# Optimization experiments

Measured on AMD Instinct MI355X. Metric: run time of the kernel, lower is better.

The kernel has to match this reference:

```python
import jax, jax.numpy as jnp
import numpy as np
import math

NUM_HEADS = 16
VEC_SIZE = 1024
HEAD_DIM = VEC_SIZE // NUM_HEADS


def setup_inputs() -> dict:
    key = jax.random.key(0)
    k1, k2, k3, k4, k5 = jax.random.split(key, 5)
    B, S, D = 2, 2048, VEC_SIZE
    x = jax.random.normal(k1, (B, S, D), dtype=jnp.float32)
    # Linear params, torch-style: y = x @ W.T + b
    s1 = 1.0 / math.sqrt(D)
    W_qkv = jax.random.uniform(k2, (3 * D, D), minval=-s1, maxval=s1, dtype=jnp.float32)
    b_qkv = jax.random.uniform(k3, (3 * D,), minval=-s1, maxval=s1, dtype=jnp.float32)
    W_out = jax.random.uniform(k4, (D, D), minval=-s1, maxval=s1, dtype=jnp.float32)
    b_out = jax.random.uniform(k5, (D,), minval=-s1, maxval=s1, dtype=jnp.float32)
    return {"x": x, "W_qkv": W_qkv, "b_qkv": b_qkv, "W_out": W_out, "b_out": b_out}


def reference(x, W_qkv, b_qkv, W_out, b_out):
    B, S, D = x.shape
    H, Hd = NUM_HEADS, HEAD_DIM
    qkv = x @ W_qkv.T + b_qkv                      # [B,S,3D]
    q, k, v = jnp.split(qkv, 3, axis=-1)
    # [B,S,H,Hd] -> [B,H,S,Hd]
    q = q.reshape(B, S, H, Hd).transpose(0, 2, 1, 3)
    k = k.reshape(B, S, H, Hd).transpose(0, 2, 1, 3)
    v = v.reshape(B, S, H, Hd).transpose(0, 2, 1, 3)
    weight = jnp.einsum('bhqd,bhkd->bhqk', q, k)   # [B,H,S,S]
    causal = jnp.triu(jnp.ones((S, S), dtype=bool), k=1)
    weight = jnp.where(causal, -jnp.inf, weight)
    weight = weight / jnp.sqrt(jnp.asarray(Hd, dtype=weight.dtype))
    weight = jax.nn.softmax(weight, axis=-1)
    out = jnp.einsum('bhqk,bhkd->bhqd', weight, v)  # [B,H,S,Hd]
    out = out.transpose(0, 2, 1, 3).reshape(B, S, D)
    return out @ W_out.T + b_out
```

## Files before the change

kernel.cpp:

```cpp
#include <hip/hip_runtime.h>
#include <hip/hip_bf16.h>

typedef __attribute__((ext_vector_type(8))) short short8;
typedef __attribute__((ext_vector_type(4))) short s4v;
typedef __attribute__((ext_vector_type(4))) float floatx4;

__device__ inline floatx4 mfma_bf16(short8 a, short8 b, floatx4 c) {
  return __builtin_amdgcn_mfma_f32_16x16x32_bf16(a, b, c, 0, 0, 0);
}
__device__ inline float exp2_fast(float x) { return __builtin_amdgcn_exp2f(x); }

__device__ inline short bf16s(float f) {
  __hip_bfloat16 h = __float2bfloat16(f);
  return *reinterpret_cast<short*>(&h);
}
__device__ inline float sbf16(short s) {
  return __bfloat162float(*reinterpret_cast<__hip_bfloat16*>(&s));
}

__device__ inline void gld16(__hip_bfloat16* lds, const __hip_bfloat16* g) {
  __builtin_amdgcn_global_load_lds(
      (const __attribute__((address_space(1))) void*)g,
      (__attribute__((address_space(3))) void*)lds, 16, 0, 0);
}

__global__ __launch_bounds__(256) void cvt_all(
    const float* __restrict__ x, const float* __restrict__ wqkv,
    const float* __restrict__ wout, __hip_bfloat16* __restrict__ xb,
    __hip_bfloat16* __restrict__ wqkvb, __hip_bfloat16* __restrict__ wob) {
  const int n1 = 4194304, n2 = 3145728;
  int i = (blockIdx.x * 256 + threadIdx.x) * 8;
  const float* src;
  __hip_bfloat16* dst;
  int off;
  if (i < n1) { src = x; dst = xb; off = i; }
  else if (i < n1 + n2) { src = wqkv; dst = wqkvb; off = i - n1; }
  else { src = wout; dst = wob; off = i - n1 - n2; }
  float4 a = *reinterpret_cast<const float4*>(src + off);
  float4 b = *reinterpret_cast<const float4*>(src + off + 4);
  __hip_bfloat16 t[8];
  t[0] = __float2bfloat16(a.x); t[1] = __float2bfloat16(a.y);
  t[2] = __float2bfloat16(a.z); t[3] = __float2bfloat16(a.w);
  t[4] = __float2bfloat16(b.x); t[5] = __float2bfloat16(b.y);
  t[6] = __float2bfloat16(b.z); t[7] = __float2bfloat16(b.w);
  *reinterpret_cast<short8*>(dst + off) = *reinterpret_cast<short8*>(t);
}

template<int TN, bool OUT_BF16>
__global__ __launch_bounds__(256) void gemm_bt(
    const __hip_bfloat16* __restrict__ A, const __hip_bfloat16* __restrict__ Bt,
    const float* __restrict__ bias, void* __restrict__ Cout,
    int M, int N, int K) {
  __shared__ __align__(16) __hip_bfloat16 As[128 * 64];
  __shared__ __align__(16) __hip_bfloat16 Bs[TN * 64];
  const int tid = threadIdx.x;
  const int wave = tid >> 6, lane = tid & 63, quad = lane >> 4, l15 = lane & 15;
  const int wm = (wave >> 1) * 64, wn = (wave & 1) * (TN / 2);
  const int m0 = blockIdx.y * 128, n0 = blockIdx.x * TN;
  const int NC = TN / 32;

  floatx4 acc[4][NC];
  for (int r = 0; r < 4; ++r)
    for (int c = 0; c < NC; ++c) acc[r][c] = (floatx4){0.f, 0.f, 0.f, 0.f};

  for (int k0 = 0; k0 < K; k0 += 64) {
    __syncthreads();
    for (int it = 0; it < 4; ++it) {
      int idx = it * 256 + tid;
      int row = idx >> 3, col = ((idx & 7) ^ (row & 7)) * 8;
      gld16(&As[idx * 8], A + (size_t)(m0 + row) * K + k0 + col);
    }
    for (int it = 0; it < TN * 64 / 2048; ++it) {
      int idx = it * 256 + tid;
      int row = idx >> 3, col = ((idx & 7) ^ (row & 7)) * 8;
      gld16(&Bs[idx * 8], Bt + (size_t)(n0 + row) * K + k0 + col);
    }
    __syncthreads();
    for (int ks = 0; ks < 2; ++ks) {
      short8 af[4], bf[NC];
      for (int r = 0; r < 4; ++r) {
        int row = wm + r * 16 + l15;
        af[r] = *reinterpret_cast<const short8*>(
            &As[row * 64 + (((ks * 4 + quad) ^ (l15 & 7)) * 8)]);
      }
      for (int c = 0; c < NC; ++c) {
        int row = wn + c * 16 + l15;
        bf[c] = *reinterpret_cast<const short8*>(
            &Bs[row * 64 + (((ks * 4 + quad) ^ (l15 & 7)) * 8)]);
      }
      for (int r = 0; r < 4; ++r)
        for (int c = 0; c < NC; ++c)
          acc[r][c] = mfma_bf16(af[r], bf[c], acc[r][c]);
    }
  }

  for (int c = 0; c < NC; ++c) {
    int gn = n0 + wn + c * 16 + l15;
    float bv = bias[gn];
    for (int r = 0; r < 4; ++r)
      for (int rg = 0; rg < 4; ++rg) {
        int gm = m0 + wm + r * 16 + quad * 4 + rg;
        float v = acc[r][c][rg] + bv;
        if (OUT_BF16)
          ((__hip_bfloat16*)Cout)[(size_t)gm * N + gn] = __float2bfloat16(v);
        else
          ((float*)Cout)[(size_t)gm * N + gn] = v;
      }
  }
}

__device__ inline void stage_half(__hip_bfloat16* lds, const __hip_bfloat16* g,
                                  int K, int tid) {
#pragma unroll
  for (int it = 0; it < 2; ++it) {
    int idx = it * 512 + tid;
    int row = idx >> 3, col = ((idx & 7) ^ (row & 7)) * 8;
    gld16(lds + idx * 8, g + (size_t)row * K + col);
  }
}

#define PHASE(MH, NH, STAGE_STMT, VM)                                          \
  do {                                                                         \
    if (NH == 0) {                                                             \
      _Pragma("unroll") for (int mf = 0; mf < 4; ++mf) {                       \
        int rh = wm * 64 + mf * 16 + l15;                                      \
        _Pragma("unroll") for (int ks = 0; ks < 2; ++ks)                       \
            af[mf][ks] = *reinterpret_cast<const short8*>(                     \
                &SA[cb][MH][rh * 64 + (((ks * 4 + quad) ^ (rh & 7)) * 8)]);    \
      }                                                                        \
    }                                                                          \
    _Pragma("unroll") for (int nf = 0; nf < 2; ++nf) {                         \
      int rh = wn * 32 + nf * 16 + l15;                                        \
      _Pragma("unroll") for (int ks = 0; ks < 2; ++ks)                         \
          bf[nf][ks] = *reinterpret_cast<const short8*>(                       \
              &SB[cb][NH][rh * 64 + (((ks * 4 + quad) ^ (rh & 7)) * 8)]);      \
    }                                                                          \
    STAGE_STMT;                                                                \
    __builtin_amdgcn_s_barrier();                                              \
    __builtin_amdgcn_s_setprio(1);                                             \
    _Pragma("unroll") for (int mf = 0; mf < 4; ++mf)                           \
        _Pragma("unroll") for (int nf = 0; nf < 2; ++nf) {                     \
      acc[MH][NH][mf][nf] = mfma_bf16(af[mf][0], bf[nf][0], acc[MH][NH][mf][nf]); \
      acc[MH][NH][mf][nf] = mfma_bf16(af[mf][1], bf[nf][1], acc[MH][NH][mf][nf]); \
    }                                                                          \
    __builtin_amdgcn_s_setprio(0);                                             \
    asm volatile("s_waitcnt vmcnt(" #VM ")" ::: "memory");                     \
    __builtin_amdgcn_s_barrier();                                              \
  } while (0)

template<bool OUT_BF16>
__global__ __launch_bounds__(512, 2) void gemm_256(
    const __hip_bfloat16* __restrict__ A, const __hip_bfloat16* __restrict__ Bt,
    const float* __restrict__ bias, void* __restrict__ Cout,
    int M, int N, int K) {
  __shared__ __align__(16) __hip_bfloat16 SA[2][2][128 * 64];
  __shared__ __align__(16) __hip_bfloat16 SB[2][2][128 * 64];
  const int tid = threadIdx.x;
  const int lane = tid & 63, quad = (lane >> 4), l15 = lane & 15;
  const int wave = tid >> 6;
  const int wm = wave >> 2, wn = wave & 3;

  const int nbx = gridDim.x;
  int bid = blockIdx.y * nbx + blockIdx.x;
  const int nwg = nbx * gridDim.y;
  if ((nwg & 7) == 0) bid = (bid & 7) * (nwg >> 3) + (bid >> 3);
  const int bx = bid % nbx, by = bid / nbx;
  const int m0 = by * 256, n0 = bx * 256;

  const __hip_bfloat16* Abase = A + (size_t)m0 * K;
  const __hip_bfloat16* Bbase = Bt + (size_t)n0 * K;
  const int NT = K >> 6;

  floatx4 acc[2][2][4][2];
#pragma unroll
  for (int a = 0; a < 2; ++a)
#pragma unroll
    for (int b = 0; b < 2; ++b)
#pragma unroll
      for (int c = 0; c < 4; ++c)
#pragma unroll
        for (int d = 0; d < 2; ++d) acc[a][b][c][d] = (floatx4){0.f, 0.f, 0.f, 0.f};

  short8 af[4][2];
  short8 bf[2][2];

  stage_half(&SA[0][0][0], Abase, K, tid);
  stage_half(&SB[0][0][0], Bbase, K, tid);
  stage_half(&SB[0][1][0], Bbase + (size_t)128 * K, K, tid);
  stage_half(&SA[0][1][0], Abase + (size_t)128 * K, K, tid);
  asm volatile("s_waitcnt vmcnt(4)" ::: "memory");
  __builtin_amdgcn_s_barrier();

  for (int t = 0; t < NT - 1; ++t) {
    const int cb = t & 1, nb = cb ^ 1;
    const int k1 = (t + 1) * 64;
    PHASE(0, 0, stage_half(&SA[nb][0][0], Abase + k1, K, tid), 4);
    PHASE(0, 1, stage_half(&SB[nb][0][0], Bbase + k1, K, tid), 4);
    PHASE(1, 0, stage_half(&SB[nb][1][0], Bbase + (size_t)128 * K + k1, K, tid), 4);
    PHASE(1, 1, stage_half(&SA[nb][1][0], Abase + (size_t)128 * K + k1, K, tid), 4);
  }
  {
    const int cb = (NT - 1) & 1;
    PHASE(0, 0, (void)0, 2);
    PHASE(0, 1, (void)0, 0);
    PHASE(1, 0, (void)0, 0);
    PHASE(1, 1, (void)0, 0);
  }

#pragma unroll
  for (int nh = 0; nh < 2; ++nh)
#pragma unroll
    for (int nf = 0; nf < 2; ++nf) {
      int gn = n0 + nh * 128 + wn * 32 + nf * 16 + l15;
      float bv = bias[gn];
#pragma unroll
      for (int mh = 0; mh < 2; ++mh)
#pragma unroll
        for (int mf = 0; mf < 4; ++mf)
#pragma unroll
          for (int rg = 0; rg < 4; ++rg) {
            int gm = m0 + mh * 128 + wm * 64 + mf * 16 + quad * 4 + rg;
            float v = acc[mh][nh][mf][nf][rg] + bv;
            if (OUT_BF16)
              ((__hip_bfloat16*)Cout)[(size_t)gm * N + gn] = __float2bfloat16(v);
            else
              ((float*)Cout)[(size_t)gm * N + gn] = v;
          }
    }
}

__global__ __launch_bounds__(256, 4) void flash_attn(
    const __hip_bfloat16* __restrict__ qkv, __hip_bfloat16* __restrict__ out) {
  const int S = 2048, QKV = 3072;
  const int bx = blockIdx.x;
  const int g = (blockIdx.y >> 3) + 2 * blockIdx.z;
  int qt;
  if (g == 0)      qt = bx;
  else if (g == 1) qt = 31 - bx;
  else if (g == 2) qt = (bx + 8) & 31;
  else             qt = (23 - bx) & 31;
  const int h = blockIdx.y, b = blockIdx.z;
  const int q0 = qt * 64;
  __shared__ __align__(16) short Ps[2][64 * 64];
  const int tid = threadIdx.x;
  const int wave = tid >> 6, lane = tid & 63, quad = lane >> 4, l15 = lane & 15;
  const int rx = l15 & 7;
  const __hip_bfloat16* base = qkv + (size_t)b * S * QKV;
  const float c2 = 0.18033688011112042f;
  const floatx4 zero4 = {0.f, 0.f, 0.f, 0.f};
  const int krow = 16 * wave + l15;

  const __hip_bfloat16* kbase = base + 1024 + h * 64;
  const __hip_bfloat16* vbase = base + 2048 + h * 64;

  for (int it = 0; it < 2; ++it) {
    int v = tid + it * 256;
    int row = v >> 3, cb = v & 7;
    int colp = (cb ^ (row & 7)) * 8;
    short8 qv = *reinterpret_cast<const short8*>(
        base + (size_t)(q0 + row) * QKV + h * 64 + cb * 8);
    short qs[8];
    for (int e = 0; e < 8; ++e) qs[e] = bf16s(sbf16(qv[e]) * c2);
    *reinterpret_cast<short8*>(&Ps[1][row * 64 + colp]) = *reinterpret_cast<short8*>(qs);
  }
  short8 kA0 = *reinterpret_cast<const short8*>(
      kbase + (size_t)krow * QKV + quad * 8);
  short8 kA1 = *reinterpret_cast<const short8*>(
      kbase + (size_t)krow * QKV + 32 + quad * 8);
  __syncthreads();

  short8 aq[4][2];
  for (int t4 = 0; t4 < 4; ++t4)
    for (int s = 0; s < 2; ++s)
      aq[t4][s] = *reinterpret_cast<const short8*>(
          &Ps[1][(t4 * 16 + l15) * 64 + (((s * 4 + quad) ^ rx) * 8)]);

  floatx4 o_acc[4];
  for (int m = 0; m < 4; ++m) o_acc[m] = zero4;
  float lsum4[4] = {0.f, 0.f, 0.f, 0.f};
  short8 vA0, vA1;

  for (int j = 0; j <= qt; ++j) {
    const int cj = j & 1, pj = cj ^ 1;

    short8 kB0, kB1, vB0, vB1;
    if (j < qt) {
      const __hip_bfloat16* kp = kbase + (size_t)((j + 1) * 64 + krow) * QKV;
      kB0 = *reinterpret_cast<const short8*>(kp + quad * 8);
      kB1 = *reinterpret_cast<const short8*>(kp + 32 + quad * 8);
    }
    {
      const __hip_bfloat16* vp = vbase + (size_t)(j * 64 + quad * 8) * QKV + krow;
      for (int i = 0; i < 8; ++i) {
        vB0[i] = *reinterpret_cast<const short*>(vp + (size_t)i * QKV);
        vB1[i] = *reinterpret_cast<const short*>(vp + (size_t)(32 + i) * QKV);
      }
    }

    if (j > 0) {
      for (int s = 0; s < 2; ++s) {
        short8 bv = s ? vA1 : vA0;
        for (int m = 0; m < 4; ++m) {
          short8 ap = *reinterpret_cast<const short8*>(
              &Ps[pj][(m * 16 + l15) * 64 + (((4 * s + quad) ^ rx) * 8)]);
          o_acc[m] = mfma_bf16(ap, bv, o_acc[m]);
        }
      }
    }

    floatx4 sc[4];
    for (int t4 = 0; t4 < 4; ++t4) {
      sc[t4] = mfma_bf16(kA0, aq[t4][0], zero4);
      sc[t4] = mfma_bf16(kA1, aq[t4][1], sc[t4]);
    }
    if (j == qt) {
      int kloc = 16 * wave + quad * 4;
      for (int t4 = 0; t4 < 4; ++t4)
        for (int rg = 0; rg < 4; ++rg)
          if (kloc + rg > t4 * 16 + l15) sc[t4][rg] = -1e30f;
    }

    const int pcol = ((2 * wave + (quad >> 1)) ^ rx) * 8 + (quad & 1) * 4;
    for (int t4 = 0; t4 < 4; ++t4) {
      short pp[4];
      for (int rg = 0; rg < 4; ++rg) {
        float p = exp2_fast(sc[t4][rg]);
        lsum4[t4] += p;
        pp[rg] = bf16s(p);
      }
      *reinterpret_cast<s4v*>(&Ps[cj][(t4 * 16 + l15) * 64 + pcol]) =
          *reinterpret_cast<s4v*>(pp);
    }

    kA0 = kB0; kA1 = kB1; vA0 = vB0; vA1 = vB1;
    __syncthreads();
  }

  const int pq = qt & 1;
  for (int s = 0; s < 2; ++s) {
    short8 bv = s ? vA1 : vA0;
    for (int m = 0; m < 4; ++m) {
      short8 ap = *reinterpret_cast<const short8*>(
          &Ps[pq][(m * 16 + l15) * 64 + (((4 * s + quad) ^ rx) * 8)]);
      o_acc[m] = mfma_bf16(ap, bv, o_acc[m]);
    }
  }
  for (int t4 = 0; t4 < 4; ++t4) {
    lsum4[t4] += __shfl_xor(lsum4[t4], 16);
    lsum4[t4] += __shfl_xor(lsum4[t4], 32);
  }
  float* Lf = (float*)&Ps[pq ^ 1][0];
  if (quad == 0)
    for (int t4 = 0; t4 < 4; ++t4)
      Lf[wave * 64 + t4 * 16 + l15] = lsum4[t4];
  __syncthreads();
  if (tid < 64)
    Lf[256 + tid] = 1.0f / (Lf[tid] + Lf[64 + tid] + Lf[128 + tid] + Lf[192 + tid]);
  __syncthreads();

  const int dcol = h * 64 + krow;
  for (int m = 0; m < 4; ++m)
    for (int rg = 0; rg < 4; ++rg) {
      int q = m * 16 + quad * 4 + rg;
      out[(size_t)(b * S + q0 + q) * 1024 + dcol] =
          __float2bfloat16(o_acc[m][rg] * Lf[256 + q]);
    }
}

extern "C" void kernel_launch(void* const* d_in, const int* in_sizes, int n_in,
                              void* d_out, int out_size, void* d_ws, size_t ws_size,
                              hipStream_t stream) {
  const float* x    = (const float*)d_in[0];
  const float* Wqkv = (const float*)d_in[1];
  const float* bqkv = (const float*)d_in[2];
  const float* Wout = (const float*)d_in[3];
  const float* bout = (const float*)d_in[4];
  float* out = (float*)d_out;

  const int BS = 2 * 2048;
  const int D = 1024;
  char* ws = (char*)d_ws;
  __hip_bfloat16* xb    = (__hip_bfloat16*)(ws);
  __hip_bfloat16* wqkvb = (__hip_bfloat16*)(ws + (size_t)8  * 1048576);
  __hip_bfloat16* wob   = (__hip_bfloat16*)(ws + (size_t)14 * 1048576);
  __hip_bfloat16* qkvb  = (__hip_bfloat16*)(ws + (size_t)16 * 1048576);
  __hip_bfloat16* attnb = (__hip_bfloat16*)(ws + (size_t)40 * 1048576);

  cvt_all<<<4096, 256, 0, stream>>>(x, Wqkv, Wout, xb, wqkvb, wob);

  gemm_256<true><<<dim3(3072 / 256, BS / 256), 512, 0, stream>>>(
      xb, wqkvb, bqkv, qkvb, BS, 3 * D, D);

  flash_attn<<<dim3(32, 16, 2), 256, 0, stream>>>(qkvb, attnb);

  gemm_bt<64, false><<<dim3(1024 / 64, BS / 128), 256, 0, stream>>>(
      attnb, wob, bout, out, BS, D, D);
}
```

Measured before the change: 177.3 us.

## Deepen gemm_256 prefetch pipeline and use it for output projection

Restructures the LDS staging schedule in gemm_256 so tiles for k+2 are prefetched into the just-consumed half-buffers, with fewer vmcnt waits per iteration, adding a peeled tail. Also replaces the simple gemm_bt kernel for the output projection with gemm_256 (256x256 tiles, 512 threads). The output GEMM grid shrinks to 64 blocks, which may underfill the GPU's compute units, trading occupancy for per-block efficiency.

```diff
diff --git a/kernel.cpp b/kernel.cpp
--- a/kernel.cpp
+++ b/kernel.cpp
@@ -46,69 +46,6 @@
   *reinterpret_cast<short8*>(dst + off) = *reinterpret_cast<short8*>(t);
 }
 
-template<int TN, bool OUT_BF16>
-__global__ __launch_bounds__(256) void gemm_bt(
-    const __hip_bfloat16* __restrict__ A, const __hip_bfloat16* __restrict__ Bt,
-    const float* __restrict__ bias, void* __restrict__ Cout,
-    int M, int N, int K) {
-  __shared__ __align__(16) __hip_bfloat16 As[128 * 64];
-  __shared__ __align__(16) __hip_bfloat16 Bs[TN * 64];
-  const int tid = threadIdx.x;
-  const int wave = tid >> 6, lane = tid & 63, quad = lane >> 4, l15 = lane & 15;
-  const int wm = (wave >> 1) * 64, wn = (wave & 1) * (TN / 2);
-  const int m0 = blockIdx.y * 128, n0 = blockIdx.x * TN;
-  const int NC = TN / 32;
-
-  floatx4 acc[4][NC];
-  for (int r = 0; r < 4; ++r)
-    for (int c = 0; c < NC; ++c) acc[r][c] = (floatx4){0.f, 0.f, 0.f, 0.f};
-
-  for (int k0 = 0; k0 < K; k0 += 64) {
-    __syncthreads();
-    for (int it = 0; it < 4; ++it) {
-      int idx = it * 256 + tid;
-      int row = idx >> 3, col = ((idx & 7) ^ (row & 7)) * 8;
-      gld16(&As[idx * 8], A + (size_t)(m0 + row) * K + k0 + col);
-    }
-    for (int it = 0; it < TN * 64 / 2048; ++it) {
-      int idx = it * 256 + tid;
-      int row = idx >> 3, col = ((idx & 7) ^ (row & 7)) * 8;
-      gld16(&Bs[idx * 8], Bt + (size_t)(n0 + row) * K + k0 + col);
-    }
-    __syncthreads();
-    for (int ks = 0; ks < 2; ++ks) {
-      short8 af[4], bf[NC];
-      for (int r = 0; r < 4; ++r) {
-        int row = wm + r * 16 + l15;
-        af[r] = *reinterpret_cast<const short8*>(
-            &As[row * 64 + (((ks * 4 + quad) ^ (l15 & 7)) * 8)]);
-      }
-      for (int c = 0; c < NC; ++c) {
-        int row = wn + c * 16 + l15;
-        bf[c] = *reinterpret_cast<const short8*>(
-            &Bs[row * 64 + (((ks * 4 + quad) ^ (l15 & 7)) * 8)]);
-      }
-      for (int r = 0; r < 4; ++r)
-        for (int c = 0; c < NC; ++c)
-          acc[r][c] = mfma_bf16(af[r], bf[c], acc[r][c]);
-    }
-  }
-
-  for (int c = 0; c < NC; ++c) {
-    int gn = n0 + wn + c * 16 + l15;
-    float bv = bias[gn];
-    for (int r = 0; r < 4; ++r)
-      for (int rg = 0; rg < 4; ++rg) {
-        int gm = m0 + wm + r * 16 + quad * 4 + rg;
-        float v = acc[r][c][rg] + bv;
-        if (OUT_BF16)
-          ((__hip_bfloat16*)Cout)[(size_t)gm * N + gn] = __float2bfloat16(v);
-        else
-          ((float*)Cout)[(size_t)gm * N + gn] = v;
-      }
-  }
-}
-
 __device__ inline void stage_half(__hip_bfloat16* lds, const __hip_bfloat16* g,
                                   int K, int tid) {
 #pragma unroll
@@ -119,7 +56,9 @@
   }
 }
 
-#define PHASE(MH, NH, STAGE_STMT, VM)                                          \
+#define VMW(N) asm volatile("s_waitcnt vmcnt(" #N ")" ::: "memory")
+
+#define PHASE(MH, NH, STAGE_STMT, WAIT_STMT)                                   \
   do {                                                                         \
     if (NH == 0) {                                                             \
       _Pragma("unroll") for (int mf = 0; mf < 4; ++mf) {                       \
@@ -144,7 +83,7 @@
       acc[MH][NH][mf][nf] = mfma_bf16(af[mf][1], bf[nf][1], acc[MH][NH][mf][nf]); \
     }                                                                          \
     __builtin_amdgcn_s_setprio(0);                                             \
-    asm volatile("s_waitcnt vmcnt(" #VM ")" ::: "memory");                     \
+    WAIT_STMT;                                                                 \
     __builtin_amdgcn_s_barrier();                                              \
   } while (0)
 
@@ -186,25 +125,39 @@
 
   stage_half(&SA[0][0][0], Abase, K, tid);
   stage_half(&SB[0][0][0], Bbase, K, tid);
+  stage_half(&SA[0][1][0], Abase + (size_t)128 * K, K, tid);
   stage_half(&SB[0][1][0], Bbase + (size_t)128 * K, K, tid);
-  stage_half(&SA[0][1][0], Abase + (size_t)128 * K, K, tid);
-  asm volatile("s_waitcnt vmcnt(4)" ::: "memory");
+  stage_half(&SA[1][0][0], Abase + 64, K, tid);
+  stage_half(&SA[1][1][0], Abase + (size_t)128 * K + 64, K, tid);
+  stage_half(&SB[1][0][0], Bbase + 64, K, tid);
+  VMW(10);
   __builtin_amdgcn_s_barrier();
 
-  for (int t = 0; t < NT - 1; ++t) {
+  for (int t = 0; t <= NT - 3; ++t) {
     const int cb = t & 1, nb = cb ^ 1;
-    const int k1 = (t + 1) * 64;
-    PHASE(0, 0, stage_half(&SA[nb][0][0], Abase + k1, K, tid), 4);
-    PHASE(0, 1, stage_half(&SB[nb][0][0], Bbase + k1, K, tid), 4);
-    PHASE(1, 0, stage_half(&SB[nb][1][0], Bbase + (size_t)128 * K + k1, K, tid), 4);
-    PHASE(1, 1, stage_half(&SA[nb][1][0], Abase + (size_t)128 * K + k1, K, tid), 4);
+    const size_t k1 = (size_t)(t + 1) * 64, k2 = (size_t)(t + 2) * 64;
+    PHASE(0, 0, stage_half(&SB[nb][1][0], Bbase + (size_t)128 * K + k1, K, tid), VMW(8));
+    PHASE(0, 1, stage_half(&SA[cb][0][0], Abase + k2, K, tid), (void)0);
+    PHASE(1, 0, (void)0, (void)0);
+    PHASE(1, 1,
+          { stage_half(&SA[cb][1][0], Abase + (size_t)128 * K + k2, K, tid);
+            stage_half(&SB[cb][0][0], Bbase + k2, K, tid); },
+          VMW(8));
+  }
+  {
+    const int cb = (NT - 2) & 1, nb = cb ^ 1;
+    const size_t k1 = (size_t)(NT - 1) * 64;
+    PHASE(0, 0, stage_half(&SB[nb][1][0], Bbase + (size_t)128 * K + k1, K, tid), VMW(8));
+    PHASE(0, 1, (void)0, (void)0);
+    PHASE(1, 0, (void)0, (void)0);
+    PHASE(1, 1, (void)0, VMW(2));
   }
   {
     const int cb = (NT - 1) & 1;
-    PHASE(0, 0, (void)0, 2);
-    PHASE(0, 1, (void)0, 0);
-    PHASE(1, 0, (void)0, 0);
-    PHASE(1, 1, (void)0, 0);
+    PHASE(0, 0, (void)0, VMW(0));
+    PHASE(0, 1, (void)0, (void)0);
+    PHASE(1, 0, (void)0, (void)0);
+    PHASE(1, 1, (void)0, (void)0);
   }
 
 #pragma unroll
@@ -393,6 +346,6 @@
 
   flash_attn<<<dim3(32, 16, 2), 256, 0, stream>>>(qkvb, attnb);
 
-  gemm_bt<64, false><<<dim3(1024 / 64, BS / 128), 256, 0, stream>>>(
+  gemm_256<false><<<dim3(1024 / 256, BS / 256), 512, 0, stream>>>(
       attnb, wob, bout, out, BS, D, D);
 }
```

New measurement: 188.2 us. +6.2%, slower.

## Deepen GEMM pipeline: prefetch two K-tiles ahead and double-buffer LDS fragments

Applied to the files above, without the earlier changes.

Restructures the 256x256 bf16 GEMM main loop so global→LDS loads run two K-steps ahead instead of one. LDS→register fragment reads for the next phase are issued alongside the current phase's MFMAs using separate register sets (af0/af1, bf0c/bf0n/bf1). The quadrant order is also changed to a snake (00,01,11,10) to reuse fragments. This aims to hide global load latency and LDS read latency behind MFMA work. In exchange it raises register pressure at 2 blocks/CU and adds more explicit waitcnt bookkeeping.

```diff
diff --git a/kernel.cpp b/kernel.cpp
--- a/kernel.cpp
+++ b/kernel.cpp
@@ -119,33 +119,47 @@
   }
 }
 
-#define PHASE(MH, NH, STAGE_STMT, VM)                                          \
+#define VMW(N) asm volatile("s_waitcnt vmcnt(" #N ")" ::: "memory")
+#define LGKM0 asm volatile("s_waitcnt lgkmcnt(0)" ::: "memory")
+#define BAR __builtin_amdgcn_s_barrier()
+
+#define LDA8(dst, BUF, MH)                                                     \
   do {                                                                         \
-    if (NH == 0) {                                                             \
-      _Pragma("unroll") for (int mf = 0; mf < 4; ++mf) {                       \
-        int rh = wm * 64 + mf * 16 + l15;                                      \
-        _Pragma("unroll") for (int ks = 0; ks < 2; ++ks)                       \
-            af[mf][ks] = *reinterpret_cast<const short8*>(                     \
-                &SA[cb][MH][rh * 64 + (((ks * 4 + quad) ^ (rh & 7)) * 8)]);    \
-      }                                                                        \
+    _Pragma("unroll") for (int mf = 0; mf < 4; ++mf) {                         \
+      int rh = wm * 64 + mf * 16 + l15;                                        \
+      _Pragma("unroll") for (int ks = 0; ks < 2; ++ks)                         \
+          dst[mf][ks] = *reinterpret_cast<const short8*>(                      \
+              &SA[BUF][MH][rh * 64 + (((ks * 4 + quad) ^ (rh & 7)) * 8)]);     \
     }                                                                          \
+  } while (0)
+#define LDB4(dst, BUF, NH)                                                     \
+  do {                                                                         \
     _Pragma("unroll") for (int nf = 0; nf < 2; ++nf) {                         \
       int rh = wn * 32 + nf * 16 + l15;                                        \
       _Pragma("unroll") for (int ks = 0; ks < 2; ++ks)                         \
-          bf[nf][ks] = *reinterpret_cast<const short8*>(                       \
-              &SB[cb][NH][rh * 64 + (((ks * 4 + quad) ^ (rh & 7)) * 8)]);      \
+          dst[nf][ks] = *reinterpret_cast<const short8*>(                      \
+              &SB[BUF][NH][rh * 64 + (((ks * 4 + quad) ^ (rh & 7)) * 8)]);     \
     }                                                                          \
-    STAGE_STMT;                                                                \
-    __builtin_amdgcn_s_barrier();                                              \
-    __builtin_amdgcn_s_setprio(1);                                             \
+  } while (0)
+#define MM16(MH, NH, AF, BF)                                                   \
+  do {                                                                         \
     _Pragma("unroll") for (int mf = 0; mf < 4; ++mf)                           \
         _Pragma("unroll") for (int nf = 0; nf < 2; ++nf) {                     \
-      acc[MH][NH][mf][nf] = mfma_bf16(af[mf][0], bf[nf][0], acc[MH][NH][mf][nf]); \
-      acc[MH][NH][mf][nf] = mfma_bf16(af[mf][1], bf[nf][1], acc[MH][NH][mf][nf]); \
+      acc[MH][NH][mf][nf] = mfma_bf16(AF[mf][0], BF[nf][0], acc[MH][NH][mf][nf]); \
+      acc[MH][NH][mf][nf] = mfma_bf16(AF[mf][1], BF[nf][1], acc[MH][NH][mf][nf]); \
     }                                                                          \
+  } while (0)
+#define PH(RD, STG, MH, NH, AF, BF, WT)                                        \
+  do {                                                                         \
+    RD;                                                                        \
+    STG;                                                                       \
+    BAR;                                                                       \
+    __builtin_amdgcn_s_setprio(1);                                             \
+    MM16(MH, NH, AF, BF);                                                      \
     __builtin_amdgcn_s_setprio(0);                                             \
-    asm volatile("s_waitcnt vmcnt(" #VM ")" ::: "memory");                     \
-    __builtin_amdgcn_s_barrier();                                              \
+    WT;                                                                        \
+    LGKM0;                                                                     \
+    BAR;                                                                       \
   } while (0)
 
 template<bool OUT_BF16>
@@ -181,30 +195,63 @@
 #pragma unroll
         for (int d = 0; d < 2; ++d) acc[a][b][c][d] = (floatx4){0.f, 0.f, 0.f, 0.f};
 
-  short8 af[4][2];
-  short8 bf[2][2];
-
+  short8 af0[4][2], af1[4][2];
+  short8 bf0c[2][2], bf0n[2][2];
+  short8 bf1[2][2];
+
+  stage_half(&SB[0][0][0], Bbase, K, tid);
   stage_half(&SA[0][0][0], Abase, K, tid);
-  stage_half(&SB[0][0][0], Bbase, K, tid);
   stage_half(&SB[0][1][0], Bbase + (size_t)128 * K, K, tid);
   stage_half(&SA[0][1][0], Abase + (size_t)128 * K, K, tid);
-  asm volatile("s_waitcnt vmcnt(4)" ::: "memory");
-  __builtin_amdgcn_s_barrier();
-
-  for (int t = 0; t < NT - 1; ++t) {
+  stage_half(&SB[1][0][0], Bbase + 64, K, tid);
+  stage_half(&SA[1][0][0], Abase + 64, K, tid);
+  stage_half(&SB[1][1][0], Bbase + (size_t)128 * K + 64, K, tid);
+  stage_half(&SA[1][1][0], Abase + (size_t)128 * K + 64, K, tid);
+  VMW(12);
+  BAR;
+  LDB4(bf0c, 0, 0);
+  LDA8(af0, 0, 0);
+  VMW(10);
+  LGKM0;
+  BAR;
+
+  for (int t = 0; t <= NT - 3; ++t) {
     const int cb = t & 1, nb = cb ^ 1;
-    const int k1 = (t + 1) * 64;
-    PHASE(0, 0, stage_half(&SA[nb][0][0], Abase + k1, K, tid), 4);
-    PHASE(0, 1, stage_half(&SB[nb][0][0], Bbase + k1, K, tid), 4);
-    PHASE(1, 0, stage_half(&SB[nb][1][0], Bbase + (size_t)128 * K + k1, K, tid), 4);
-    PHASE(1, 1, stage_half(&SA[nb][1][0], Abase + (size_t)128 * K + k1, K, tid), 4);
+    const size_t k2 = (size_t)(t + 2) * 64;
+    PH(LDB4(bf1, cb, 1), stage_half(&SB[cb][0][0], Bbase + k2, K, tid),
+       0, 0, af0, bf0c, VMW(10));
+    PH(LDA8(af1, cb, 1), stage_half(&SA[cb][0][0], Abase + k2, K, tid),
+       0, 1, af0, bf1, VMW(10));
+    PH(LDB4(bf0n, nb, 0),
+       stage_half(&SB[cb][1][0], Bbase + (size_t)128 * K + k2, K, tid),
+       1, 1, af1, bf1, VMW(10));
+    PH(LDA8(af0, nb, 0),
+       stage_half(&SA[cb][1][0], Abase + (size_t)128 * K + k2, K, tid),
+       1, 0, af1, bf0c, VMW(10));
+#pragma unroll
+    for (int nf = 0; nf < 2; ++nf)
+#pragma unroll
+      for (int ks = 0; ks < 2; ++ks) bf0c[nf][ks] = bf0n[nf][ks];
+  }
+  {
+    const int cb = (NT - 2) & 1, nb = cb ^ 1;
+    PH(LDB4(bf1, cb, 1), (void)0, 0, 0, af0, bf0c, VMW(8));
+    PH(LDA8(af1, cb, 1), (void)0, 0, 1, af0, bf1, VMW(6));
+    PH(LDB4(bf0n, nb, 0), (void)0, 1, 1, af1, bf1, VMW(4));
+    PH(LDA8(af0, nb, 0), (void)0, 1, 0, af1, bf0c, VMW(2));
+#pragma unroll
+    for (int nf = 0; nf < 2; ++nf)
+#pragma unroll
+      for (int ks = 0; ks < 2; ++ks) bf0c[nf][ks] = bf0n[nf][ks];
   }
   {
     const int cb = (NT - 1) & 1;
-    PHASE(0, 0, (void)0, 2);
-    PHASE(0, 1, (void)0, 0);
-    PHASE(1, 0, (void)0, 0);
-    PHASE(1, 1, (void)0, 0);
+    PH(LDB4(bf1, cb, 1), (void)0, 0, 0, af0, bf0c, VMW(0));
+    PH(LDA8(af1, cb, 1), (void)0, 0, 1, af0, bf1, (void)0);
+    __builtin_amdgcn_s_setprio(1);
+    MM16(1, 1, af1, bf1);
+    MM16(1, 0, af1, bf0c);
+    __builtin_amdgcn_s_setprio(0);
   }
 
 #pragma unroll
```

After: 197.6 us. 1.11x slower.
